# Kernel optimization log

Measured on AMD Instinct MI355X. Metric: run time of the kernel, lower is better.

The kernel has to match this reference:

```python
import jax, jax.numpy as jnp
import numpy as np

N, E, H, L, R, NG = 8192, 131072, 256, 3, 128, 64
NUM_ELEMENTS = 80
CUTOFF = 12.0
INV_SQRT_2 = 1.0 / np.sqrt(2.0)
INV_SQRT_3 = 1.0 / np.sqrt(3.0)
INV_SQRT_H = 1.0 / np.sqrt(H)


def _glorot(key, shape):
    fan_in, fan_out = shape[-2], shape[-1]
    return jax.random.normal(key, shape, jnp.float32) * np.sqrt(2.0 / (fan_in + fan_out))


def setup_inputs():
    key = jax.random.key(0)
    ks = jax.random.split(key, 24)
    pos = jax.random.normal(ks[0], (N, 3), jnp.float32) * 5.0
    z = jax.random.randint(ks[1], (N,), 0, NUM_ELEMENTS)
    src = jax.random.randint(ks[2], (E,), 0, N)
    off = jax.random.randint(ks[3], (E,), 1, N)
    dst = (src + off) % N  # guarantee no self-loops (dist > 0)
    edge_index = jnp.stack([src, dst])
    batch = jnp.sort(jax.random.randint(ks[4], (N,), 0, NG))
    return {
        "pos": pos,
        "atom_emb": jax.random.normal(ks[5], (NUM_ELEMENTS, H), jnp.float32),
        "ln_w": jnp.ones((L, H), jnp.float32),
        "ln_b": jnp.zeros((L, H), jnp.float32),
        "xp_w1": _glorot(ks[6], (L, H, H)),
        "xp_b1": jnp.zeros((L, H), jnp.float32),
        "xp_w2": _glorot(ks[7], (L, H, 3 * H)),
        "xp_b2": jnp.zeros((L, 3 * H), jnp.float32),
        "rbf_w": _glorot(ks[8], (L, R, 3 * H)),
        "rbf_b": jnp.zeros((L, 3 * H), jnp.float32),
        "vec_w": _glorot(ks[9], (L, H, 2 * H)),
        "xv_w1": _glorot(ks[10], (L, 2 * H, H)),
        "xv_b1": jnp.zeros((L, H), jnp.float32),
        "xv_w2": _glorot(ks[11], (L, H, 3 * H)),
        "xv_b2": jnp.zeros((L, 3 * H), jnp.float32),
        "oe_w1": _glorot(ks[12], (H, H // 2)),
        "oe_b1": jnp.zeros((H // 2,), jnp.float32),
        "oe_w2": _glorot(ks[13], (H // 2, 1)),
        "oe_b2": jnp.zeros((1,), jnp.float32),
        "z": z,
        "edge_index": edge_index,
        "batch": batch,
    }


def _gaussian_rbf(dist):
    offset = jnp.linspace(0.0, CUTOFF, R)
    coeff = -0.5 / (offset[1] - offset[0]) ** 2
    return jnp.exp(coeff * (dist[:, None] - offset[None, :]) ** 2)  # [E, R]


def _layernorm(x, w, b):
    mu = x.mean(-1, keepdims=True)
    var = x.var(-1, keepdims=True)
    return (x - mu) / jnp.sqrt(var + 1e-5) * w + b


def reference(pos, atom_emb, ln_w, ln_b, xp_w1, xp_b1, xp_w2, xp_b2,
              rbf_w, rbf_b, vec_w, xv_w1, xv_b1, xv_w2, xv_b2,
              oe_w1, oe_b1, oe_w2, oe_b2, z, edge_index, batch):
    src, dst = edge_index[0], edge_index[1]
    rel = pos[src] - pos[dst]                       # [E, 3]
    dist = jnp.sqrt((rel ** 2).sum(-1))             # [E]
    edge_rbf = _gaussian_rbf(dist)                  # [E, R]
    edge_vector = rel / dist[:, None]               # [E, 3] unit vectors

    x = atom_emb[z]                                 # [N, H]
    vec = jnp.zeros((N, 3, H), x.dtype)

    for l in range(L):
        # ---- PaiNNMessage ----
        xh = _layernorm(x, ln_w[l], ln_b[l])
        xh = jax.nn.silu(xh @ xp_w1[l] + xp_b1[l]) @ xp_w2[l] + xp_b2[l]  # [N, 3H]
        rbfh = edge_rbf @ rbf_w[l] + rbf_b[l]                             # [E, 3H]
        m = xh[src] * rbfh
        mx, xh2, xh3 = jnp.split(m, 3, axis=-1)
        xh2 = xh2 * INV_SQRT_3
        mvec = (vec[src] * xh2[:, None, :] + xh3[:, None, :] * edge_vector[:, :, None]) * INV_SQRT_H
        dx = jax.ops.segment_sum(mx, dst, num_segments=N)
        dvec = jax.ops.segment_sum(mvec, dst, num_segments=N)
        x = (x + dx) * INV_SQRT_2
        vec = vec + dvec

        # ---- PaiNNUpdate ----
        vp = vec @ vec_w[l]                          # [N, 3, 2H]
        vec1, vec2 = jnp.split(vp, 2, axis=-1)
        vec_dot = (vec1 * vec2).sum(axis=1) * INV_SQRT_H           # [N, H]
        vnorm = jnp.sqrt((vec2 ** 2).sum(axis=1) + 1e-8)           # [N, H]
        h = jnp.concatenate([x, vnorm], axis=-1)
        h = jax.nn.silu(h @ xv_w1[l] + xv_b1[l]) @ xv_w2[l] + xv_b2[l]
        xv1, xv2, xv3 = jnp.split(h, 3, axis=-1)
        dx = (xv1 + xv2 * vec_dot) * INV_SQRT_2
        dvec = xv3[:, None, :] * vec1
        x = (x + dx) * INV_SQRT_2
        vec = vec + dvec

    # ---- energy head: per-atom MLP then per-molecule sum ----
    per_atom = jax.nn.silu(x @ oe_w1 + oe_b1) @ oe_w2 + oe_b2      # [N, 1]
    energy = jax.ops.segment_sum(per_atom, batch, num_segments=NG)  # [NG, 1]
    return energy
```

## Files before the change

### kernel.cpp

```cpp
#include <hip/hip_runtime.h>
#include <hip/hip_bf16.h>
#include <math.h>

#define NN 8192
#define EE 131072
#define HH 256
#define LL 3
#define RR 128
#define NGG 64
#define MSG_WAVES 16
#define CHUNK 16

typedef __attribute__((ext_vector_type(8))) short bf16x8;
typedef __attribute__((ext_vector_type(4))) float f32x4;
typedef unsigned short u16;

#if defined(__has_builtin)
#if __has_builtin(__builtin_amdgcn_fdot2_f32_bf16)
#define HAVE_FDOT2 1
typedef __attribute__((ext_vector_type(2))) __bf16 bf16x2_t;
union BU { unsigned u; bf16x2_t v; };
#endif
#if __has_builtin(__builtin_amdgcn_global_load_lds)
#define HAVE_GLL 1
#endif
#endif

union U4 { ushort4 v; unsigned short a[4]; };
union U8 { uint4 v; unsigned short a[8]; unsigned w[4]; };

__device__ __forceinline__ float silu(float v) { return v / (1.0f + expf(-v)); }
__device__ __forceinline__ float b2f(unsigned short u) { return __uint_as_float(((unsigned)u) << 16); }
__device__ __forceinline__ unsigned short f2b(float f) {
    unsigned u = __float_as_uint(f);
    u += 0x7fff + ((u >> 16) & 1);
    return (unsigned short)(u >> 16);
}

constexpr float kInvSqrt2 = 0.70710678118654752440f;
constexpr float kInvSqrt3 = 0.57735026918962576451f;
constexpr float kInvSqrtH = 0.0625f;

__global__ void k_zero(float* __restrict__ p, int n4) {
    int i = blockIdx.x * 256 + threadIdx.x;
    if (i < n4) ((float4*)p)[i] = make_float4(0.f, 0.f, 0.f, 0.f);
}

__global__ __launch_bounds__(256) void k_wt_all(
    const float* __restrict__ xp_w1, const float* __restrict__ xp_w2,
    const float* __restrict__ rbf_w, const float* __restrict__ vec_w,
    const float* __restrict__ xv_w1, const float* __restrict__ xv_w2,
    const float* __restrict__ oe_w1,
    u16* __restrict__ xp_w1T, u16* __restrict__ xp_w2T, u16* __restrict__ rbf_wP,
    u16* __restrict__ vec_wT, u16* __restrict__ xv_w1T, u16* __restrict__ xv_w2T,
    u16* __restrict__ oe_w1T) {
    int bid = blockIdx.x;
    const float* src; u16* dst; int K, N, t, pairmode = 0;
    if (bid < 2400) {
        int l = bid / 800, r = bid % 800;
        if (r < 64)       { src = xp_w1 + (size_t)l * 65536;  dst = xp_w1T + (size_t)l * 65536;  K = 256; N = 256; t = r; }
        else if (r < 256) { src = xp_w2 + (size_t)l * 196608; dst = xp_w2T + (size_t)l * 196608; K = 256; N = 768; t = r - 64; }
        else if (r < 352) { src = rbf_w + (size_t)l * 98304;  dst = rbf_wP + (size_t)l * 98304;  K = 128; N = 768; t = r - 256; pairmode = 1; }
        else if (r < 480) { src = vec_w + (size_t)l * 131072; dst = vec_wT + (size_t)l * 131072; K = 256; N = 512; t = r - 352; }
        else if (r < 608) { src = xv_w1 + (size_t)l * 131072; dst = xv_w1T + (size_t)l * 131072; K = 512; N = 256; t = r - 480; }
        else              { src = xv_w2 + (size_t)l * 196608; dst = xv_w2T + (size_t)l * 196608; K = 256; N = 768; t = r - 608; }
    } else {
        src = oe_w1; dst = oe_w1T; K = 256; N = 128; t = bid - 2400;
    }
    int nx = N >> 5;
    int bn = (t % nx) * 32, bk = (t / nx) * 32;
    int tx = threadIdx.x & 31, ty = threadIdx.x >> 5;
    if (pairmode) {
#pragma unroll
        for (int i = 0; i < 32; i += 8) {
            int k = bk + ty + i, n = bn + tx;
            dst[(size_t)(k >> 1) * 1536 + n * 2 + (k & 1)] = f2b(src[(size_t)k * N + n]);
        }
        return;
    }
    __shared__ float tile[32][33];
#pragma unroll
    for (int i = 0; i < 32; i += 8)
        tile[ty + i][tx] = src[(size_t)(bk + ty + i) * N + bn + tx];
    __syncthreads();
#pragma unroll
    for (int i = 0; i < 32; i += 8)
        dst[(size_t)(bn + ty + i) * K + bk + tx] = f2b(tile[tx][ty + i]);
}

__global__ void k_init_ln(const float* __restrict__ emb, const int* __restrict__ z,
                          const float* __restrict__ w, const float* __restrict__ b,
                          float* __restrict__ x, u16* __restrict__ xlnb) {
    int n = blockIdx.x, t = threadIdx.x;
    float v = emb[z[n] * HH + t];
    x[(size_t)n * HH + t] = v;
    float s = v, q = v * v;
#pragma unroll
    for (int m = 32; m >= 1; m >>= 1) {
        s += __shfl_xor(s, m, 64);
        q += __shfl_xor(q, m, 64);
    }
    __shared__ float s_sum[4], s_sq[4];
    int wid = t >> 6;
    if ((t & 63) == 0) { s_sum[wid] = s; s_sq[wid] = q; }
    __syncthreads();
    float S = s_sum[0] + s_sum[1] + s_sum[2] + s_sum[3];
    float Q = s_sq[0] + s_sq[1] + s_sq[2] + s_sq[3];
    float mu = S * (1.0f / HH);
    float var = Q * (1.0f / HH) - mu * mu;
    float rs = rsqrtf(var + 1e-5f);
    xlnb[(size_t)n * HH + t] = f2b((v - mu) * rs * w[t] + b[t]);
}

__global__ void k_geom_hist(const float* __restrict__ pos, const int* __restrict__ ei,
                            float* __restrict__ ev, int* __restrict__ deg) {
    int e = blockIdx.x * 256 + threadIdx.x;
    if (e >= EE) return;
    int s = ei[e], d = ei[EE + e];
    float rx = pos[s * 3 + 0] - pos[d * 3 + 0];
    float ry = pos[s * 3 + 1] - pos[d * 3 + 1];
    float rz = pos[s * 3 + 2] - pos[d * 3 + 2];
    float dist = sqrtf(rx * rx + ry * ry + rz * rz);
    float inv = 1.0f / dist;
    ((float4*)ev)[e] = make_float4(rx * inv, ry * inv, rz * inv, dist);
    atomicAdd(&deg[d], 1);
}

__global__ void k_scan(const int* __restrict__ deg, int* __restrict__ row_ptr,
                       int* __restrict__ fill) {
    __shared__ int buf[256];
    __shared__ int carry_s;
    int t = threadIdx.x;
    if (t == 0) carry_s = 0;
    __syncthreads();
    for (int r = 0; r < NN; r += 256) {
        int v = deg[r + t];
        buf[t] = v;
        __syncthreads();
        for (int ofs = 1; ofs < 256; ofs <<= 1) {
            int add = (t >= ofs) ? buf[t - ofs] : 0;
            __syncthreads();
            buf[t] += add;
            __syncthreads();
        }
        int excl = buf[t] - v;
        int carry = carry_s;
        row_ptr[r + t] = carry + excl;
        fill[r + t] = carry + excl;
        __syncthreads();
        if (t == 255) carry_s = carry + buf[t];
        __syncthreads();
    }
    if (t == 0) row_ptr[NN] = carry_s;
}

__global__ void k_scatter(const int* __restrict__ ei, const float* __restrict__ ev,
                          int* __restrict__ fill, int* __restrict__ srcp,
                          float4* __restrict__ evp, int* __restrict__ kptab,
                          unsigned* __restrict__ gtab, int* __restrict__ dstp) {
    int e = blockIdx.x * 256 + threadIdx.x;
    if (e >= EE) return;
    int d = ei[EE + e];
    int pos = atomicAdd(&fill[d], 1);
    float4 e4 = ((const float4*)ev)[e];
    srcp[pos] = ei[e];
    dstp[pos] = d;
    evp[pos] = e4;
    const float step = 12.0f / 127.0f;
    const float coeff = -0.5f / (step * step);
    float dist = e4.w;
    int k0 = ((int)floorf(dist / step) - 3) & ~1;
    k0 = k0 < 0 ? 0 : (k0 > 120 ? 120 : k0);
    float g[8];
#pragma unroll
    for (int k = 0; k < 8; ++k) {
        float t = dist - (k0 + k) * step;
        g[k] = expf(coeff * t * t);
    }
    kptab[pos] = k0 >> 1;
    unsigned g0 = (unsigned)f2b(g[0]) | ((unsigned)f2b(g[1]) << 16);
    unsigned g1 = (unsigned)f2b(g[2]) | ((unsigned)f2b(g[3]) << 16);
    unsigned g2 = (unsigned)f2b(g[4]) | ((unsigned)f2b(g[5]) << 16);
    unsigned g3 = (unsigned)f2b(g[6]) | ((unsigned)f2b(g[7]) << 16);
    ((uint4*)gtab)[pos] = make_uint4(g0, g1, g2, g3);
}

template <int OUT_BF16, int ACT>
__global__ __launch_bounds__(256) void k_gemm(
    const u16* __restrict__ A, const u16* __restrict__ BT,
    const float* __restrict__ bias, void* __restrict__ C, int M, int K, int N) {
    __shared__ u16 As[4096];
    __shared__ u16 Bs[4096];
    int tid = threadIdx.x;
    int wave = tid >> 6, lane = tid & 63;
    int bm = blockIdx.y * 128, bn = blockIdx.x * 128;
    int wm = (wave >> 1) * 64, wn = (wave & 1) * 64;
    int lm = lane & 15;
    int kg = lane >> 4;
    f32x4 acc[4][4] = {};

    for (int k0 = 0; k0 < K; k0 += 32) {
#pragma unroll
        for (int it = 0; it < 2; ++it) {
            int idx = it * 256 + tid;
            int r = idx >> 2, seg = idx & 3;
#ifdef HAVE_GLL
            __builtin_amdgcn_global_load_lds(
                (const unsigned*)&A[(size_t)(bm + r) * K + k0 + seg * 8],
                (unsigned*)&As[idx * 8], 16, 0, 0);
            __builtin_amdgcn_global_load_lds(
                (const unsigned*)&BT[(size_t)(bn + r) * K + k0 + seg * 8],
                (unsigned*)&Bs[idx * 8], 16, 0, 0);
#else
            *(uint4*)&As[idx * 8] = *(const uint4*)&A[(size_t)(bm + r) * K + k0 + seg * 8];
            *(uint4*)&Bs[idx * 8] = *(const uint4*)&BT[(size_t)(bn + r) * K + k0 + seg * 8];
#endif
        }
        __syncthreads();
        bf16x8 af[4], bfr[4];
#pragma unroll
        for (int i = 0; i < 4; ++i)
            af[i] = *(const bf16x8*)&As[(wm + i * 16 + lm) * 32 + kg * 8];
#pragma unroll
        for (int j = 0; j < 4; ++j)
            bfr[j] = *(const bf16x8*)&Bs[(wn + j * 16 + lm) * 32 + kg * 8];
#pragma unroll
        for (int i = 0; i < 4; ++i)
#pragma unroll
            for (int j = 0; j < 4; ++j)
                acc[i][j] = __builtin_amdgcn_mfma_f32_16x16x32_bf16(af[i], bfr[j], acc[i][j], 0, 0, 0);
        __syncthreads();
    }

#pragma unroll
    for (int j = 0; j < 4; ++j) {
        int col = bn + wn + j * 16 + lm;
        float bv = bias ? bias[col] : 0.f;
#pragma unroll
        for (int i = 0; i < 4; ++i) {
            int row0 = bm + wm + i * 16 + kg * 4;
#pragma unroll
            for (int r = 0; r < 4; ++r) {
                float v = acc[i][j][r] + bv;
                if (ACT) v = silu(v);
                if (OUT_BF16)
                    ((u16*)C)[(size_t)(row0 + r) * N + col] = f2b(v);
                else
                    ((float*)C)[(size_t)(row0 + r) * N + col] = v;
            }
        }
    }
}

__global__ __launch_bounds__(1024) void k_msg(
    const u16* __restrict__ xhb, const u16* __restrict__ vinb,
    const int* __restrict__ srcp, const float4* __restrict__ evp,
    const int* __restrict__ dstp, const int* __restrict__ kptab,
    const unsigned* __restrict__ gtab, const u16* __restrict__ WP ,
    const float* __restrict__ rbias,
    float* __restrict__ accX, float* __restrict__ accV,
    float* __restrict__ bufA, float* __restrict__ bufB) {
    __shared__ u16 Wp[64 * 512];
    int tid = threadIdx.x;
    int wave = tid >> 6, lane = tid & 63;
    int c0 = lane * 4;
    int gw = blockIdx.x * MSG_WAVES + wave;
    int E0 = gw * CHUNK, E1 = E0 + CHUNK;
    float* bA = bufA + (size_t)gw * 1024;
    float* bB = bufB + (size_t)gw * 1024;

#pragma unroll
    for (int p = 0; p < 3; ++p) {
        __syncthreads();
#pragma unroll
        for (int it = 0; it < 4; ++it) {
            int idx = it * 1024 + tid;
            int r = idx >> 6;
            int c8 = (idx & 63) * 8;
            *(uint4*)&Wp[r * 512 + c8] =
                *(const uint4*)&WP[(size_t)r * 1536 + p * 512 + c8];
        }
        __syncthreads();
        float4 bb = ((const float4*)(rbias + p * 256))[lane];
        float bias4[4] = {bb.x, bb.y, bb.z, bb.w};
        float acc[3][4] = {};
        int dcur = dstp[E0];
        int rs = E0;
        auto flush = [&](int dn, int rstart, int atEnd) {
            int isFirst = (rstart == E0);
            if (p == 0) {
                float* q = isFirst ? bA : (atEnd ? bB : accX + (size_t)dn * 256);
                *(float4*)&q[c0] = make_float4(acc[0][0], acc[0][1], acc[0][2], acc[0][3]);
            } else {
                float* q = isFirst ? bA + 256 : (atEnd ? bB + 256 : accV + (size_t)dn * 768);
                if (p == 1) {
#pragma unroll
                    for (int k = 0; k < 3; ++k)
                        *(float4*)&q[k * 256 + c0] =
                            make_float4(acc[k][0], acc[k][1], acc[k][2], acc[k][3]);
                } else {
#pragma unroll
                    for (int k = 0; k < 3; ++k) {
                        float4 o = *(const float4*)&q[k * 256 + c0];
                        o.x += acc[k][0]; o.y += acc[k][1];
                        o.z += acc[k][2]; o.w += acc[k][3];
                        *(float4*)&q[k * 256 + c0] = o;
                    }
                }
            }
#pragma unroll
            for (int k = 0; k < 3; ++k)
#pragma unroll
                for (int c = 0; c < 4; ++c) acc[k][c] = 0.f;
        };
#pragma unroll 2
        for (int j = E0; j < E1; ++j) {
            int d = dstp[j];
            if (d != dcur) { flush(dcur, rs, 0); dcur = d; rs = j; }
            int s = srcp[j];
            int kp = kptab[j];
            uint4 gt = ((const uint4*)gtab)[j];
            unsigned gp[4] = {gt.x, gt.y, gt.z, gt.w};
            float rr[4] = {bias4[0], bias4[1], bias4[2], bias4[3]};
#pragma unroll
            for (int p2 = 0; p2 < 4; ++p2) {
                U8 w;
                w.v = *(const uint4*)&Wp[(kp + p2) * 512 + c0 * 2];
#ifdef HAVE_FDOT2
                BU gv; gv.u = gp[p2];
#pragma unroll
                for (int c = 0; c < 4; ++c) {
                    BU wv; wv.u = w.w[c];
                    rr[c] = __builtin_amdgcn_fdot2_f32_bf16(wv.v, gv.v, rr[c], false);
                }
#else
                float ge = b2f((u16)(gp[p2] & 0xffff));
                float go = b2f((u16)(gp[p2] >> 16));
#pragma unroll
                for (int c = 0; c < 4; ++c)
                    rr[c] += ge * b2f(w.a[2 * c]) + go * b2f(w.a[2 * c + 1]);
#endif
            }
            if (p == 0) {
                U4 X; X.v = *(const ushort4*)(xhb + (size_t)s * 768 + c0);
#pragma unroll
                for (int c = 0; c < 4; ++c) acc[0][c] += b2f(X.a[c]) * rr[c];
            } else if (p == 1) {
                U4 X, V0, V1, V2;
                X.v = *(const ushort4*)(xhb + (size_t)s * 768 + 256 + c0);
                V0.v = *(const ushort4*)(vinb + (size_t)s * 768 + c0);
                V1.v = *(const ushort4*)(vinb + (size_t)s * 768 + 256 + c0);
                V2.v = *(const ushort4*)(vinb + (size_t)s * 768 + 512 + c0);
#pragma unroll
                for (int c = 0; c < 4; ++c) {
                    float m1 = b2f(X.a[c]) * rr[c] * kInvSqrt3;
                    acc[0][c] += b2f(V0.a[c]) * m1;
                    acc[1][c] += b2f(V1.a[c]) * m1;
                    acc[2][c] += b2f(V2.a[c]) * m1;
                }
            } else {
                U4 X; X.v = *(const ushort4*)(xhb + (size_t)s * 768 + 512 + c0);
                float4 ev4 = evp[j];
#pragma unroll
                for (int c = 0; c < 4; ++c) {
                    float m2 = b2f(X.a[c]) * rr[c];
                    acc[0][c] += m2 * ev4.x;
                    acc[1][c] += m2 * ev4.y;
                    acc[2][c] += m2 * ev4.z;
                }
            }
        }
        flush(dcur, rs, 1);
    }
}

__global__ void k_msg_epi(const int* __restrict__ row_ptr,
                          const float* __restrict__ accX, const float* __restrict__ accV,
                          const float* __restrict__ bufA, const float* __restrict__ bufB,
                          float* __restrict__ x, const float* __restrict__ vin,
                          u16* __restrict__ vecMb) {
    int n = blockIdx.x, t = threadIdx.x;
    int e0 = row_ptr[n], e1 = row_ptr[n + 1];
    float ax = 0.f, av0 = 0.f, av1 = 0.f, av2 = 0.f;
    if (e1 > e0) {
        int w0 = e0 >> 4, w1 = (e1 - 1) >> 4;
        bool direct = (w0 == w1) && ((e0 & (CHUNK - 1)) != 0) && ((e1 & (CHUNK - 1)) != 0);
        if (direct) {
            ax  = accX[(size_t)n * 256 + t];
            av0 = accV[(size_t)n * 768 + t];
            av1 = accV[(size_t)n * 768 + 256 + t];
            av2 = accV[(size_t)n * 768 + 512 + t];
        } else {
            const float* q = ((e0 & (CHUNK - 1)) == 0) ? bufA + (size_t)w0 * 1024
                                                       : bufB + (size_t)w0 * 1024;
            ax  += q[t];
            av0 += q[256 + t];
            av1 += q[512 + t];
            av2 += q[768 + t];
            for (int w = w0 + 1; w <= w1; ++w) {
                const float* r = bufA + (size_t)w * 1024;
                ax  += r[t];
                av0 += r[256 + t];
                av1 += r[512 + t];
                av2 += r[768 + t];
            }
        }
    }
    size_t xi = (size_t)n * 256 + t;
    float nx = (x[xi] + ax) * kInvSqrt2;
    x[xi] = nx;
    size_t vi = (size_t)n * 768 + t;
    vecMb[vi]       = f2b(vin[vi]       + av0 * kInvSqrtH);
    vecMb[vi + 256] = f2b(vin[vi + 256] + av1 * kInvSqrtH);
    vecMb[vi + 512] = f2b(vin[vi + 512] + av2 * kInvSqrtH);
}

__global__ void k_vecdot(const u16* __restrict__ vp, const float* __restrict__ x,
                         float* __restrict__ vec_dot, u16* __restrict__ hcat) {
    int i = blockIdx.x * 256 + threadIdx.x;
    int n = i >> 8, c = i & 255;
    const u16* p = vp + (size_t)n * 1536;
    float dsum = 0.f, qsum = 0.f;
#pragma unroll
    for (int k = 0; k < 3; ++k) {
        float v1 = b2f(p[k * 512 + c]);
        float v2 = b2f(p[k * 512 + 256 + c]);
        dsum += v1 * v2;
        qsum += v2 * v2;
    }
    vec_dot[i] = dsum * kInvSqrtH;
    hcat[(size_t)n * 512 + c] = f2b(x[i]);
    hcat[(size_t)n * 512 + 256 + c] = f2b(sqrtf(qsum + 1e-8f));
}

__global__ void k_update_out(const u16* __restrict__ hout, const float* __restrict__ vec_dot,
                             const u16* __restrict__ vp, float* __restrict__ x,
                             const u16* __restrict__ vecMb, float* __restrict__ vfin,
                             u16* __restrict__ vb,
                             const float* __restrict__ lnw, const float* __restrict__ lnb,
                             u16* __restrict__ xout) {
    int n = blockIdx.x, t = threadIdx.x;
    size_t i = (size_t)n * 256 + t;
    float xv1 = b2f(hout[(size_t)n * 768 + t]);
    float xv2 = b2f(hout[(size_t)n * 768 + 256 + t]);
    float xv3 = b2f(hout[(size_t)n * 768 + 512 + t]);
    float dxv = (xv1 + xv2 * vec_dot[i]) * kInvSqrt2;
    float nx = (x[i] + dxv) * kInvSqrt2;
    x[i] = nx;
#pragma unroll
    for (int k = 0; k < 3; ++k) {
        size_t idx = (size_t)n * 768 + k * 256 + t;
        float nv = b2f(vecMb[idx]) + xv3 * b2f(vp[(size_t)n * 1536 + k * 512 + t]);
        vfin[idx] = nv;
        vb[idx] = f2b(nv);
    }
    if (lnw) {
        float s = nx, q = nx * nx;
#pragma unroll
        for (int m = 32; m >= 1; m >>= 1) {
            s += __shfl_xor(s, m, 64);
            q += __shfl_xor(q, m, 64);
        }
        __shared__ float s_sum[4], s_sq[4];
        int wid = t >> 6;
        if ((t & 63) == 0) { s_sum[wid] = s; s_sq[wid] = q; }
        __syncthreads();
        float S = s_sum[0] + s_sum[1] + s_sum[2] + s_sum[3];
        float Q = s_sq[0] + s_sq[1] + s_sq[2] + s_sq[3];
        float mu = S * (1.0f / HH);
        float var = Q * (1.0f / HH) - mu * mu;
        float rs = rsqrtf(var + 1e-5f);
        xout[i] = f2b((nx - mu) * rs * lnw[t] + lnb[t]);
    } else {
        xout[i] = f2b(nx);
    }
}

__global__ void k_energy2(const float* __restrict__ h, const float* __restrict__ w2,
                          const float* __restrict__ b2, const int* __restrict__ batch,
                          float* __restrict__ out) {
    __shared__ float g[NGG];
    int t = threadIdx.x;
    if (t < NGG) g[t] = 0.f;
    __syncthreads();
    int a = blockIdx.x * 256 + t;
    const float4* hr = (const float4*)(h + (size_t)a * 128);
    const float4* w4 = (const float4*)w2;
    float acc = 0.f;
#pragma unroll 8
    for (int i = 0; i < 32; ++i) {
        float4 hv = hr[i], wv = w4[i];
        acc += hv.x * wv.x + hv.y * wv.y + hv.z * wv.z + hv.w * wv.w;
    }
    acc += b2[0];
    atomicAdd(&g[batch[a]], acc);
    __syncthreads();
    if (t < NGG && g[t] != 0.f) atomicAdd(&out[t], g[t]);
}

extern "C" void kernel_launch(void* const* d_in, const int* in_sizes, int n_in,
                              void* d_out, int out_size, void* d_ws, size_t ws_size,
                              hipStream_t stream) {
    const float* pos      = (const float*)d_in[0];
    const float* atom_emb = (const float*)d_in[1];
    const float* ln_w     = (const float*)d_in[2];
    const float* ln_b     = (const float*)d_in[3];
    const float* xp_w1    = (const float*)d_in[4];
    const float* xp_b1    = (const float*)d_in[5];
    const float* xp_w2    = (const float*)d_in[6];
    const float* xp_b2    = (const float*)d_in[7];
    const float* rbf_w    = (const float*)d_in[8];
    const float* rbf_b    = (const float*)d_in[9];
    const float* vec_w    = (const float*)d_in[10];
    const float* xv_w1    = (const float*)d_in[11];
    const float* xv_b1    = (const float*)d_in[12];
    const float* xv_w2    = (const float*)d_in[13];
    const float* xv_b2    = (const float*)d_in[14];
    const float* oe_w1    = (const float*)d_in[15];
    const float* oe_b1    = (const float*)d_in[16];
    const float* oe_w2    = (const float*)d_in[17];
    const float* oe_b2    = (const float*)d_in[18];
    const int*   z        = (const int*)d_in[19];
    const int*   ei       = (const int*)d_in[20];
    const int*   batch    = (const int*)d_in[21];
    float* out = (float*)d_out;

    char* ws = (char*)d_ws;
    size_t off = 0;
    auto alloc = [&](size_t b) {
        void* p = ws + off;
        off = (off + b + 255) & ~(size_t)255;
        return p;
    };
    float*    x      = (float*)alloc((size_t)NN * HH * 4);
    float*    vecA   = (float*)alloc((size_t)NN * 768 * 4);
    u16*      vb     = (u16*)alloc((size_t)NN * 768 * 2);
    u16*      vecMb  = (u16*)alloc((size_t)NN * 768 * 2);
    u16*      xlnb   = (u16*)alloc((size_t)NN * HH * 2);
    u16*      t1b    = (u16*)alloc((size_t)NN * HH * 2);
    u16*      xhb    = (u16*)alloc((size_t)NN * 768 * 2);
    float*    vdot   = (float*)alloc((size_t)NN * HH * 4);
    u16*      vpb    = (u16*)alloc((size_t)NN * 1536 * 2);
    float*    accX   = (float*)alloc((size_t)NN * HH * 4);
    float*    bufA   = (float*)alloc((size_t)EE / CHUNK * 1024 * 4);
    float*    bufB   = (float*)alloc((size_t)EE / CHUNK * 1024 * 4);
    u16*      houtb  = (u16*)alloc((size_t)NN * 768 * 2);
    float*    ev     = (float*)alloc((size_t)EE * 4 * 4);
    int*      deg    = (int*)alloc((size_t)NN * 4);
    int*      row_ptr= (int*)alloc((size_t)(NN + 1) * 4);
    int*      fill   = (int*)alloc((size_t)NN * 4);
    int*      srcp   = (int*)alloc((size_t)EE * 4);
    int*      dstp   = (int*)alloc((size_t)EE * 4);
    float4*   evp    = (float4*)alloc((size_t)EE * 16);
    int*      kptab  = (int*)alloc((size_t)EE * 4);
    unsigned* gtab   = (unsigned*)alloc((size_t)EE * 16);
    u16* xp_w1T   = (u16*)alloc((size_t)3 * 256 * 256 * 2);
    u16* xp_w2T   = (u16*)alloc((size_t)3 * 768 * 256 * 2);
    u16* rbf_wP   = (u16*)alloc((size_t)3 * 128 * 768 * 2);
    u16* vec_wT   = (u16*)alloc((size_t)3 * 512 * 256 * 2);
    u16* xv_w1T   = (u16*)alloc((size_t)3 * 256 * 512 * 2);
    u16* xv_w2T   = (u16*)alloc((size_t)3 * 768 * 256 * 2);
    u16* oe_w1T   = (u16*)alloc((size_t)128 * 256 * 2);
    (void)ws_size;

    u16*   h1b   = t1b;
    u16*   hcatb = xhb;
    float* heng  = vdot;
    u16*   xb    = xlnb;
    float* accV  = (float*)vpb;

    k_wt_all<<<2432, 256, 0, stream>>>(xp_w1, xp_w2, rbf_w, vec_w, xv_w1, xv_w2, oe_w1,
                                       xp_w1T, xp_w2T, rbf_wP, vec_wT, xv_w1T, xv_w2T, oe_w1T);
    k_zero<<<(36 * 1024 * 1024 / 16 + 255) / 256, 256, 0, stream>>>(vecA, 36 * 1024 * 1024 / 16);
    k_zero<<<8, 256, 0, stream>>>((float*)deg, NN / 4);
    k_init_ln<<<NN, 256, 0, stream>>>(atom_emb, z, ln_w, ln_b, x, xlnb);
    k_geom_hist<<<EE / 256, 256, 0, stream>>>(pos, ei, ev, deg);
    k_scan<<<1, 256, 0, stream>>>(deg, row_ptr, fill);
    k_scatter<<<EE / 256, 256, 0, stream>>>(ei, ev, fill, srcp, evp, kptab, gtab, dstp);

    for (int l = 0; l < LL; ++l) {
        k_gemm<1, 1><<<dim3(2, NN / 128), 256, 0, stream>>>(
            xlnb, xp_w1T + (size_t)l * 256 * 256, xp_b1 + l * HH, t1b, NN, 256, 256);
        k_gemm<1, 0><<<dim3(6, NN / 128), 256, 0, stream>>>(
            t1b, xp_w2T + (size_t)l * 768 * 256, xp_b2 + l * 768, xhb, NN, 256, 768);
        k_msg<<<EE / (CHUNK * MSG_WAVES), 1024, 0, stream>>>(
            xhb, vb, srcp, evp, dstp, kptab, gtab,
            rbf_wP + (size_t)l * 128 * 768, rbf_b + l * 768, accX, accV, bufA, bufB);
        k_msg_epi<<<NN, 256, 0, stream>>>(row_ptr, accX, accV, bufA, bufB, x, vecA, vecMb);

        k_gemm<1, 0><<<dim3(4, 3 * NN / 128), 256, 0, stream>>>(
            vecMb, vec_wT + (size_t)l * 512 * 256, nullptr, vpb, 3 * NN, 256, 512);
        k_vecdot<<<NN, 256, 0, stream>>>(vpb, x, vdot, hcatb);
        k_gemm<1, 1><<<dim3(2, NN / 128), 256, 0, stream>>>(
            hcatb, xv_w1T + (size_t)l * 256 * 512, xv_b1 + l * HH, h1b, NN, 512, 256);
        k_gemm<1, 0><<<dim3(6, NN / 128), 256, 0, stream>>>(
            h1b, xv_w2T + (size_t)l * 768 * 256, xv_b2 + l * 768, houtb, NN, 256, 768);
        bool last = (l == LL - 1);
        k_update_out<<<NN, 256, 0, stream>>>(
            houtb, vdot, vpb, x, vecMb, vecA, vb,
            last ? nullptr : ln_w + (l + 1) * HH,
            last ? nullptr : ln_b + (l + 1) * HH, xlnb);
    }

    k_gemm<0, 1><<<dim3(1, NN / 128), 256, 0, stream>>>(
        xb, oe_w1T, oe_b1, heng, NN, 256, 128);
    k_zero<<<1, 256, 0, stream>>>(out, NGG / 4);
    k_energy2<<<32, 256, 0, stream>>>(heng, oe_w2, oe_b2, batch, out);
}
```

Measured before the change: 831.4 us.

## Shrink GEMM M-tile to 64 and batch edge gathers in message kernel

The GEMM tile drops from 128x128 to 64x128 rows per block, so each wave computes a 32x64 sub-tile and twice as many blocks launch, which should fill the GPU better for these small matrices at the cost of more B-tile reloads. The message kernel now preloads per-chunk src, kptab and dst indices into registers once, with dst made wave-uniform via readfirstlane. It then processes edges in groups of four, issuing all gathers and RBF dot products before the serial accumulate-and-flush step, so memory latency can overlap. This raises register pressure in a 1024-thread kernel.

```diff
diff --git a/kernel.cpp b/kernel.cpp
--- a/kernel.cpp
+++ b/kernel.cpp
@@ -189,43 +189,49 @@
 __global__ __launch_bounds__(256) void k_gemm(
     const u16* __restrict__ A, const u16* __restrict__ BT,
     const float* __restrict__ bias, void* __restrict__ C, int M, int K, int N) {
-    __shared__ u16 As[4096];
-    __shared__ u16 Bs[4096];
+    __shared__ u16 As[64 * 32];
+    __shared__ u16 Bs[128 * 32];
     int tid = threadIdx.x;
     int wave = tid >> 6, lane = tid & 63;
-    int bm = blockIdx.y * 128, bn = blockIdx.x * 128;
-    int wm = (wave >> 1) * 64, wn = (wave & 1) * 64;
+    int bm = blockIdx.y * 64, bn = blockIdx.x * 128;
+    int wm = (wave & 1) * 32, wn = (wave >> 1) * 64;
     int lm = lane & 15;
     int kg = lane >> 4;
-    f32x4 acc[4][4] = {};
+    f32x4 acc[2][4] = {};
 
     for (int k0 = 0; k0 < K; k0 += 32) {
+        {
+            int r = tid >> 2, seg = tid & 3;
+#ifdef HAVE_GLL
+            __builtin_amdgcn_global_load_lds(
+                (const unsigned*)&A[(size_t)(bm + r) * K + k0 + seg * 8],
+                (unsigned*)&As[tid * 8], 16, 0, 0);
+#else
+            *(uint4*)&As[tid * 8] = *(const uint4*)&A[(size_t)(bm + r) * K + k0 + seg * 8];
+#endif
+        }
 #pragma unroll
         for (int it = 0; it < 2; ++it) {
             int idx = it * 256 + tid;
             int r = idx >> 2, seg = idx & 3;
 #ifdef HAVE_GLL
             __builtin_amdgcn_global_load_lds(
-                (const unsigned*)&A[(size_t)(bm + r) * K + k0 + seg * 8],
-                (unsigned*)&As[idx * 8], 16, 0, 0);
-            __builtin_amdgcn_global_load_lds(
                 (const unsigned*)&BT[(size_t)(bn + r) * K + k0 + seg * 8],
                 (unsigned*)&Bs[idx * 8], 16, 0, 0);
 #else
-            *(uint4*)&As[idx * 8] = *(const uint4*)&A[(size_t)(bm + r) * K + k0 + seg * 8];
             *(uint4*)&Bs[idx * 8] = *(const uint4*)&BT[(size_t)(bn + r) * K + k0 + seg * 8];
 #endif
         }
         __syncthreads();
-        bf16x8 af[4], bfr[4];
-#pragma unroll
-        for (int i = 0; i < 4; ++i)
+        bf16x8 af[2], bfr[4];
+#pragma unroll
+        for (int i = 0; i < 2; ++i)
             af[i] = *(const bf16x8*)&As[(wm + i * 16 + lm) * 32 + kg * 8];
 #pragma unroll
         for (int j = 0; j < 4; ++j)
             bfr[j] = *(const bf16x8*)&Bs[(wn + j * 16 + lm) * 32 + kg * 8];
 #pragma unroll
-        for (int i = 0; i < 4; ++i)
+        for (int i = 0; i < 2; ++i)
 #pragma unroll
             for (int j = 0; j < 4; ++j)
                 acc[i][j] = __builtin_amdgcn_mfma_f32_16x16x32_bf16(af[i], bfr[j], acc[i][j], 0, 0, 0);
@@ -237,7 +243,7 @@
         int col = bn + wn + j * 16 + lm;
         float bv = bias ? bias[col] : 0.f;
 #pragma unroll
-        for (int i = 0; i < 4; ++i) {
+        for (int i = 0; i < 2; ++i) {
             int row0 = bm + wm + i * 16 + kg * 4;
 #pragma unroll
             for (int r = 0; r < 4; ++r) {
@@ -265,9 +271,17 @@
     int wave = tid >> 6, lane = tid & 63;
     int c0 = lane * 4;
     int gw = blockIdx.x * MSG_WAVES + wave;
-    int E0 = gw * CHUNK, E1 = E0 + CHUNK;
+    int E0 = gw * CHUNK;
     float* bA = bufA + (size_t)gw * 1024;
     float* bB = bufB + (size_t)gw * 1024;
+
+    int sA[CHUNK], kpA[CHUNK], dA[CHUNK];
+#pragma unroll
+    for (int j = 0; j < CHUNK; ++j) {
+        sA[j]  = srcp[E0 + j];
+        kpA[j] = kptab[E0 + j];
+        dA[j]  = __builtin_amdgcn_readfirstlane(dstp[E0 + j]);
+    }
 
 #pragma unroll
     for (int p = 0; p < 3; ++p) {
@@ -284,10 +298,9 @@
         float4 bb = ((const float4*)(rbias + p * 256))[lane];
         float bias4[4] = {bb.x, bb.y, bb.z, bb.w};
         float acc[3][4] = {};
-        int dcur = dstp[E0];
-        int rs = E0;
-        auto flush = [&](int dn, int rstart, int atEnd) {
-            int isFirst = (rstart == E0);
+        int rs = 0;
+        auto flushfn = [&](int dn, int rstart, int atEnd) {
+            int isFirst = (rstart == 0);
             if (p == 0) {
                 float* q = isFirst ? bA : (atEnd ? bB : accX + (size_t)dn * 256);
                 *(float4*)&q[c0] = make_float4(acc[0][0], acc[0][1], acc[0][2], acc[0][3]);
@@ -313,64 +326,76 @@
 #pragma unroll
                 for (int c = 0; c < 4; ++c) acc[k][c] = 0.f;
         };
-#pragma unroll 2
-        for (int j = E0; j < E1; ++j) {
-            int d = dstp[j];
-            if (d != dcur) { flush(dcur, rs, 0); dcur = d; rs = j; }
-            int s = srcp[j];
-            int kp = kptab[j];
-            uint4 gt = ((const uint4*)gtab)[j];
-            unsigned gp[4] = {gt.x, gt.y, gt.z, gt.w};
-            float rr[4] = {bias4[0], bias4[1], bias4[2], bias4[3]};
-#pragma unroll
-            for (int p2 = 0; p2 < 4; ++p2) {
-                U8 w;
-                w.v = *(const uint4*)&Wp[(kp + p2) * 512 + c0 * 2];
+
+#pragma unroll
+        for (int g = 0; g < CHUNK / 4; ++g) {
+            float ctr[4][4];
+            U4 Vr[4][3];
+            float4 evr[4];
+#pragma unroll
+            for (int u = 0; u < 4; ++u) {
+                int j = g * 4 + u;
+                int s = sA[j];
+                U4 X;
+                X.v = *(const ushort4*)(xhb + (size_t)s * 768 + p * 256 + c0);
+                if (p == 1) {
+                    Vr[u][0].v = *(const ushort4*)(vinb + (size_t)s * 768 + c0);
+                    Vr[u][1].v = *(const ushort4*)(vinb + (size_t)s * 768 + 256 + c0);
+                    Vr[u][2].v = *(const ushort4*)(vinb + (size_t)s * 768 + 512 + c0);
+                }
+                if (p == 2) evr[u] = evp[E0 + j];
+                uint4 gt = ((const uint4*)gtab)[E0 + j];
+                unsigned gp[4] = {gt.x, gt.y, gt.z, gt.w};
+                float rr[4] = {bias4[0], bias4[1], bias4[2], bias4[3]};
+                int kp = kpA[j];
+#pragma unroll
+                for (int p2 = 0; p2 < 4; ++p2) {
+                    U8 w;
+                    w.v = *(const uint4*)&Wp[(kp + p2) * 512 + c0 * 2];
 #ifdef HAVE_FDOT2
-                BU gv; gv.u = gp[p2];
-#pragma unroll
-                for (int c = 0; c < 4; ++c) {
-                    BU wv; wv.u = w.w[c];
-                    rr[c] = __builtin_amdgcn_fdot2_f32_bf16(wv.v, gv.v, rr[c], false);
+                    BU gv; gv.u = gp[p2];
+#pragma unroll
+                    for (int c = 0; c < 4; ++c) {
+                        BU wv; wv.u = w.w[c];
+                        rr[c] = __builtin_amdgcn_fdot2_f32_bf16(wv.v, gv.v, rr[c], false);
+                    }
+#else
+                    float ge = b2f((u16)(gp[p2] & 0xffff));
+                    float go = b2f((u16)(gp[p2] >> 16));
+#pragma unroll
+                    for (int c = 0; c < 4; ++c)
+                        rr[c] += ge * b2f(w.a[2 * c]) + go * b2f(w.a[2 * c + 1]);
+#endif
                 }
-#else
-                float ge = b2f((u16)(gp[p2] & 0xffff));
-                float go = b2f((u16)(gp[p2] >> 16));
-#pragma unroll
-                for (int c = 0; c < 4; ++c)
-                    rr[c] += ge * b2f(w.a[2 * c]) + go * b2f(w.a[2 * c + 1]);
-#endif
+                float sc = (p == 1) ? kInvSqrt3 : 1.0f;
+#pragma unroll
+                for (int c = 0; c < 4; ++c) ctr[u][c] = b2f(X.a[c]) * rr[c] * sc;
             }
-            if (p == 0) {
-                U4 X; X.v = *(const ushort4*)(xhb + (size_t)s * 768 + c0);
-#pragma unroll
-                for (int c = 0; c < 4; ++c) acc[0][c] += b2f(X.a[c]) * rr[c];
-            } else if (p == 1) {
-                U4 X, V0, V1, V2;
-                X.v = *(const ushort4*)(xhb + (size_t)s * 768 + 256 + c0);
-                V0.v = *(const ushort4*)(vinb + (size_t)s * 768 + c0);
-                V1.v = *(const ushort4*)(vinb + (size_t)s * 768 + 256 + c0);
-                V2.v = *(const ushort4*)(vinb + (size_t)s * 768 + 512 + c0);
-#pragma unroll
-                for (int c = 0; c < 4; ++c) {
-                    float m1 = b2f(X.a[c]) * rr[c] * kInvSqrt3;
-                    acc[0][c] += b2f(V0.a[c]) * m1;
-                    acc[1][c] += b2f(V1.a[c]) * m1;
-                    acc[2][c] += b2f(V2.a[c]) * m1;
-                }
-            } else {
-                U4 X; X.v = *(const ushort4*)(xhb + (size_t)s * 768 + 512 + c0);
-                float4 ev4 = evp[j];
-#pragma unroll
-                for (int c = 0; c < 4; ++c) {
-                    float m2 = b2f(X.a[c]) * rr[c];
-                    acc[0][c] += m2 * ev4.x;
-                    acc[1][c] += m2 * ev4.y;
-                    acc[2][c] += m2 * ev4.z;
+#pragma unroll
+            for (int u = 0; u < 4; ++u) {
+                int j = g * 4 + u;
+                if (j > 0 && dA[j] != dA[j - 1]) { flushfn(dA[j - 1], rs, 0); rs = j; }
+                if (p == 0) {
+#pragma unroll
+                    for (int c = 0; c < 4; ++c) acc[0][c] += ctr[u][c];
+                } else if (p == 1) {
+#pragma unroll
+                    for (int c = 0; c < 4; ++c) {
+                        acc[0][c] += b2f(Vr[u][0].a[c]) * ctr[u][c];
+                        acc[1][c] += b2f(Vr[u][1].a[c]) * ctr[u][c];
+                        acc[2][c] += b2f(Vr[u][2].a[c]) * ctr[u][c];
+                    }
+                } else {
+#pragma unroll
+                    for (int c = 0; c < 4; ++c) {
+                        acc[0][c] += ctr[u][c] * evr[u].x;
+                        acc[1][c] += ctr[u][c] * evr[u].y;
+                        acc[2][c] += ctr[u][c] * evr[u].z;
+                    }
                 }
             }
         }
-        flush(dcur, rs, 1);
+        flushfn(dA[CHUNK - 1], rs, 1);
     }
 }
 
@@ -579,21 +604,21 @@
     k_scatter<<<EE / 256, 256, 0, stream>>>(ei, ev, fill, srcp, evp, kptab, gtab, dstp);
 
     for (int l = 0; l < LL; ++l) {
-        k_gemm<1, 1><<<dim3(2, NN / 128), 256, 0, stream>>>(
+        k_gemm<1, 1><<<dim3(2, NN / 64), 256, 0, stream>>>(
             xlnb, xp_w1T + (size_t)l * 256 * 256, xp_b1 + l * HH, t1b, NN, 256, 256);
-        k_gemm<1, 0><<<dim3(6, NN / 128), 256, 0, stream>>>(
+        k_gemm<1, 0><<<dim3(6, NN / 64), 256, 0, stream>>>(
             t1b, xp_w2T + (size_t)l * 768 * 256, xp_b2 + l * 768, xhb, NN, 256, 768);
         k_msg<<<EE / (CHUNK * MSG_WAVES), 1024, 0, stream>>>(
             xhb, vb, srcp, evp, dstp, kptab, gtab,
             rbf_wP + (size_t)l * 128 * 768, rbf_b + l * 768, accX, accV, bufA, bufB);
         k_msg_epi<<<NN, 256, 0, stream>>>(row_ptr, accX, accV, bufA, bufB, x, vecA, vecMb);
 
-        k_gemm<1, 0><<<dim3(4, 3 * NN / 128), 256, 0, stream>>>(
+        k_gemm<1, 0><<<dim3(4, 3 * NN / 64), 256, 0, stream>>>(
             vecMb, vec_wT + (size_t)l * 512 * 256, nullptr, vpb, 3 * NN, 256, 512);
         k_vecdot<<<NN, 256, 0, stream>>>(vpb, x, vdot, hcatb);
-        k_gemm<1, 1><<<dim3(2, NN / 128), 256, 0, stream>>>(
+        k_gemm<1, 1><<<dim3(2, NN / 64), 256, 0, stream>>>(
             hcatb, xv_w1T + (size_t)l * 256 * 512, xv_b1 + l * HH, h1b, NN, 512, 256);
-        k_gemm<1, 0><<<dim3(6, NN / 128), 256, 0, stream>>>(
+        k_gemm<1, 0><<<dim3(6, NN / 64), 256, 0, stream>>>(
             h1b, xv_w2T + (size_t)l * 768 * 256, xv_b2 + l * 768, houtb, NN, 256, 768);
         bool last = (l == LL - 1);
         k_update_out<<<NN, 256, 0, stream>>>(
@@ -602,7 +627,7 @@
             last ? nullptr : ln_b + (l + 1) * HH, xlnb);
     }
 
-    k_gemm<0, 1><<<dim3(1, NN / 128), 256, 0, stream>>>(
+    k_gemm<0, 1><<<dim3(1, NN / 64), 256, 0, stream>>>(
         xb, oe_w1T, oe_b1, heng, NN, 256, 128);
     k_zero<<<1, 256, 0, stream>>>(out, NGG / 4);
     k_energy2<<<32, 256, 0, stream>>>(heng, oe_w2, oe_b2, batch, out);
```

New measurement: 1.075 ms. 1.29x slower.
